# Kernel optimization log

Hardware: AMD Instinct MI355X
Metric: run time of the kernel (lower is better)

Reference implementation:

```python
import jax, jax.numpy as jnp
import numpy as np

NODES = 23   # 22 players + ball per frame-graph
K = 8        # random neighbors per node
B, T = 64, 128
G = B * T            # total graphs (frames)
N = G * NODES        # total nodes
D_IN, H, RH = 16, 128, 128


def setup_inputs() -> dict:
    key = jax.random.key(0)
    ks = jax.random.split(key, 10)
    x = jax.random.normal(ks[0], (N, D_IN), jnp.float32)
    # per-graph random edges: dst = each node repeated K times, src = random node in same graph
    src_local = jax.random.randint(ks[1], (G, NODES * K), 0, NODES)
    dst_local = jnp.tile(jnp.repeat(jnp.arange(NODES), K)[None, :], (G, 1))
    off = (jnp.arange(G) * NODES)[:, None]
    edge_index = jnp.stack([(src_local + off).reshape(-1),
                            (dst_local + off).reshape(-1)]).astype(jnp.int32)
    runner_idx = jax.random.randint(ks[2], (G,), 0, NODES, dtype=jnp.int32)
    sc = lambda k, sh: (jax.random.normal(k, sh, jnp.float32) * 0.05)
    return {
        'x': x, 'edge_index': edge_index, 'runner_idx': runner_idx,
        'W1': sc(ks[3], (D_IN, H)), 'b1': jnp.zeros((H,), jnp.float32),
        'W2': sc(ks[4], (H, H)),    'b2': jnp.zeros((H,), jnp.float32),
        'W_ih': sc(ks[5], (3 * RH, H)), 'W_hh': sc(ks[6], (3 * RH, RH)),
        'b_ih': jnp.zeros((3 * RH,), jnp.float32), 'b_hh': jnp.zeros((3 * RH,), jnp.float32),
        'Wp': sc(ks[7], (RH, 2)), 'bp': jnp.zeros((2,), jnp.float32),
    }


def _gcn_conv(h, edge_index, W, b):
    # PyG GCNConv: add self-loops, symmetric normalization, scatter-sum
    h = h @ W
    loop = jnp.arange(N, dtype=edge_index.dtype)
    s = jnp.concatenate([edge_index[0], loop])
    d = jnp.concatenate([edge_index[1], loop])
    deg = jax.ops.segment_sum(jnp.ones_like(s, h.dtype), d, num_segments=N)
    dinv = jnp.where(deg > 0, jax.lax.rsqrt(deg), 0.0)
    norm = dinv[s] * dinv[d]                      # [E+N]
    out = jax.ops.segment_sum(h[s] * norm[:, None], d, num_segments=N)
    return out + b


def _gru(seq, W_ih, W_hh, b_ih, b_hh):
    # torch GRU: gates in r,z,n order
    xg = seq @ W_ih.T + b_ih                      # [B,T,3RH]
    def step(hprev, xt):
        gh = hprev @ W_hh.T + b_hh
        xr, xz, xn = jnp.split(xt, 3, axis=-1)
        hr, hz, hn = jnp.split(gh, 3, axis=-1)
        r = jax.nn.sigmoid(xr + hr)
        z = jax.nn.sigmoid(xz + hz)
        n = jnp.tanh(xn + r * hn)
        hnew = (1.0 - z) * n + z * hprev
        return hnew, hnew
    h0 = jnp.zeros((seq.shape[0], RH), seq.dtype)
    _, outs = jax.lax.scan(step, h0, jnp.swapaxes(xg, 0, 1))
    return jnp.swapaxes(outs, 0, 1)               # [B,T,RH]


def reference(x, edge_index, runner_idx, W1, b1, W2, b2,
              W_ih, W_hh, b_ih, b_hh, Wp, bp):
    h = jax.nn.relu(_gcn_conv(x, edge_index, W1, b1))
    h = jax.nn.relu(_gcn_conv(h, edge_index, W2, b2))
    # fused equivalent of the per-graph nonzero()/indexing loop:
    runner_global = jnp.arange(G, dtype=jnp.int32) * NODES + runner_idx
    seq = h[runner_global].reshape(B, T, H)       # all lengths == T, padding is a no-op
    out = _gru(seq, W_ih, W_hh, b_ih, b_hh)
    return out @ Wp + bp                          # [B,T,2]
```

## Files before the change

### kernel.cpp

```cpp
#include <hip/hip_runtime.h>
#include <hip/hip_bf16.h>
#include <math.h>

#define GG 8192
#define NODESN 23
#define KK 8
#define DIN 16
#define HH 128
#define RHH 128
#define EPG (NODESN*KK)
#define TTT 128
#define BBB 64
#define HPAD 132

#define GRU_BARRIER() asm volatile("s_waitcnt lgkmcnt(0)\n\ts_barrier" ::: "memory")

__global__ __launch_bounds__(256) void gcn_fused(
    const float* __restrict__ x, const int* __restrict__ esrc,
    const int* __restrict__ runner,
    const float* __restrict__ W1, const float* __restrict__ b1,
    const float* __restrict__ W2, const float* __restrict__ b2,
    float* __restrict__ seq)
{
    __shared__ float xs[NODESN * DIN];
    __shared__ float W1s[DIN * HH];
    __shared__ int   srcs[EPG];
    __shared__ float t1[NODESN * HH];
    __shared__ float b1s[HH];
    __shared__ float hsum[HH];
    __shared__ float red[256];

    const int g = blockIdx.x;
    const int tid = threadIdx.x;

    for (int i = tid; i < NODESN * DIN; i += 256) xs[i] = x[g * NODESN * DIN + i];
    for (int i = tid; i < DIN * HH; i += 256)     W1s[i] = W1[i];
    for (int i = tid; i < EPG; i += 256)          srcs[i] = esrc[g * EPG + i] - g * NODESN;
    if (tid < HH) b1s[tid] = b1[tid];
    __syncthreads();

    for (int idx = tid; idx < NODESN * HH; idx += 256) {
        int n = idx >> 7, j = idx & 127;
        float acc = 0.f;
        #pragma unroll
        for (int k = 0; k < DIN; k += 4) {
            float4 xv = *(const float4*)&xs[n * DIN + k];
            acc = fmaf(xv.x, W1s[(k+0)*HH + j],
                  fmaf(xv.y, W1s[(k+1)*HH + j],
                  fmaf(xv.z, W1s[(k+2)*HH + j],
                  fmaf(xv.w, W1s[(k+3)*HH + j], acc))));
        }
        t1[idx] = acc;
    }
    __syncthreads();

    const int r = runner[g];
    {
        const int j = tid & 127, sgrp = tid >> 7;
        float part = 0.f;
        for (int slot = sgrp; slot < 9; slot += 2) {
            int node = (slot < 8) ? srcs[r * KK + slot] : r;
            float acc = t1[node * HH + j];
            #pragma unroll
            for (int k = 0; k < KK; k++) acc += t1[srcs[node * KK + k] * HH + j];
            part += fmaxf(acc * (1.f / 9.f) + b1s[j], 0.f);
        }
        red[tid] = part;
    }
    __syncthreads();
    if (tid < HH) hsum[tid] = red[tid] + red[tid + 128];
    __syncthreads();

    {
        const int j = tid & 127, kh = tid >> 7;
        float acc = 0.f;
        #pragma unroll
        for (int kq = 0; kq < 16; kq++) {
            int k = kh * 64 + kq * 4;
            float4 hv = *(const float4*)&hsum[k];
            acc = fmaf(hv.x, W2[(k+0)*HH + j],
                  fmaf(hv.y, W2[(k+1)*HH + j],
                  fmaf(hv.z, W2[(k+2)*HH + j],
                  fmaf(hv.w, W2[(k+3)*HH + j], acc))));
        }
        red[tid] = acc;
    }
    __syncthreads();
    if (tid < HH)
        seq[(size_t)g * HH + tid] =
            fmaxf((red[tid] + red[tid + 128]) * (1.f / 9.f) + b2[tid], 0.f);
}

__global__ void transpose_wih(const float* __restrict__ W, float* __restrict__ WT)
{
    int idx = blockIdx.x * 256 + threadIdx.x;
    if (idx < 3 * RHH * RHH) {
        int jj = idx / RHH, kk = idx - jj * RHH;
        WT[kk * (3 * RHH) + jj] = W[idx];
    }
}

__global__ __launch_bounds__(384) void xg_kernel(
    const float* __restrict__ seq, const float* __restrict__ WT,
    const float* __restrict__ b_ih, float* __restrict__ xg)
{
    const int tid = threadIdx.x;
    const int m0 = blockIdx.x * 8;
    const float* srow = seq + (size_t)m0 * RHH;
    float acc[8];
    const float bv = b_ih[tid];
    #pragma unroll
    for (int mi = 0; mi < 8; mi++) acc[mi] = bv;
    for (int k = 0; k < RHH; k += 4) {
        float w0 = WT[(k+0)*384 + tid];
        float w1 = WT[(k+1)*384 + tid];
        float w2 = WT[(k+2)*384 + tid];
        float w3 = WT[(k+3)*384 + tid];
        #pragma unroll
        for (int mi = 0; mi < 8; mi++) {
            float4 sv = *(const float4*)(srow + mi * RHH + k);
            acc[mi] = fmaf(sv.x, w0, fmaf(sv.y, w1, fmaf(sv.z, w2, fmaf(sv.w, w3, acc[mi]))));
        }
    }
    #pragma unroll
    for (int mi = 0; mi < 8; mi++)
        xg[(size_t)(m0 + mi) * 384 + tid] = acc[mi];
}

__global__ __launch_bounds__(512, 2) void gru_kernel(
    const float* __restrict__ xg, const float* __restrict__ W_hh,
    const float* __restrict__ b_hh, const float* __restrict__ Wp,
    const float* __restrict__ bp, float* __restrict__ out)
{
    __shared__ float h_hist[(TTT + 1) * HPAD];
    __shared__ float xg_s[2][3 * RHH];

    const int b   = blockIdx.x;
    const int tid = threadIdx.x;
    const int i   = tid >> 2;
    const int q   = tid & 3;

    float wr[32], wz[32], wn[32];
    int loff[8];
    {
        const float* br = W_hh + (size_t)i * RHH + q * 32;
        const float* bz = br + (size_t)RHH * RHH;
        const float* bn = bz + (size_t)RHH * RHH;
        #pragma unroll
        for (int m = 0; m < 8; m++) {
            int p = (m + 2 * q) & 7;
            loff[m] = q * 32 + 4 * p;
            float4 v;
            v = *(const float4*)(br + 4*p); wr[4*m]=v.x; wr[4*m+1]=v.y; wr[4*m+2]=v.z; wr[4*m+3]=v.w;
            v = *(const float4*)(bz + 4*p); wz[4*m]=v.x; wz[4*m+1]=v.y; wz[4*m+2]=v.z; wz[4*m+3]=v.w;
            v = *(const float4*)(bn + 4*p); wn[4*m]=v.x; wn[4*m+1]=v.y; wn[4*m+2]=v.z; wn[4*m+3]=v.w;
        }
    }
    float bhr = 0.f, bhz = 0.f, bhn = 0.f;
    if (q == 0) { bhr = b_hh[i]; bhz = b_hh[RHH + i]; bhn = b_hh[2 * RHH + i]; }

    if (tid < RHH) h_hist[tid] = 0.f;
    const float* xbase = xg + (size_t)b * TTT * 3 * RHH;
    float xnext = 0.f;
    if (tid < 3 * RHH) {
        xg_s[0][tid] = xbase[tid];
        xnext = xbase[3 * RHH + tid];
    }
    float hprev = 0.f;
    __syncthreads();

    for (int t = 0; t < TTT; t++) {
        const float* hrow = &h_hist[t * HPAD];
        float ar0 = 0.f, ar1 = 0.f, az0 = 0.f, az1 = 0.f, an0 = 0.f, an1 = 0.f;
        #pragma unroll
        for (int m = 0; m < 8; m++) {
            float4 hv = *(const float4*)(hrow + loff[m]);
            if (m & 1) {
                ar1 = fmaf(hv.x, wr[4*m], fmaf(hv.y, wr[4*m+1], fmaf(hv.z, wr[4*m+2], fmaf(hv.w, wr[4*m+3], ar1))));
                az1 = fmaf(hv.x, wz[4*m], fmaf(hv.y, wz[4*m+1], fmaf(hv.z, wz[4*m+2], fmaf(hv.w, wz[4*m+3], az1))));
                an1 = fmaf(hv.x, wn[4*m], fmaf(hv.y, wn[4*m+1], fmaf(hv.z, wn[4*m+2], fmaf(hv.w, wn[4*m+3], an1))));
            } else {
                ar0 = fmaf(hv.x, wr[4*m], fmaf(hv.y, wr[4*m+1], fmaf(hv.z, wr[4*m+2], fmaf(hv.w, wr[4*m+3], ar0))));
                az0 = fmaf(hv.x, wz[4*m], fmaf(hv.y, wz[4*m+1], fmaf(hv.z, wz[4*m+2], fmaf(hv.w, wz[4*m+3], az0))));
                an0 = fmaf(hv.x, wn[4*m], fmaf(hv.y, wn[4*m+1], fmaf(hv.z, wn[4*m+2], fmaf(hv.w, wn[4*m+3], an0))));
            }
        }
        float ar = ar0 + ar1, az = az0 + az1, an = an0 + an1;

        if (tid < 3 * RHH) {
            xg_s[(t + 1) & 1][tid] = xnext;
            xnext = (t + 2 < TTT) ? xbase[(size_t)(t + 2) * 3 * RHH + tid] : 0.f;
        }

        ar += __shfl_xor(ar, 1); ar += __shfl_xor(ar, 2);
        az += __shfl_xor(az, 1); az += __shfl_xor(az, 2);
        an += __shfl_xor(an, 1); an += __shfl_xor(an, 2);

        if (q == 0) {
            const float* xr_s = xg_s[t & 1];
            float xr = xr_s[i], xz = xr_s[RHH + i], xn = xr_s[2 * RHH + i];
            float sr = xr + ar + bhr;
            float sz = xz + az + bhz;
            float rg = 1.f / (1.f + __expf(-sr));
            float zg = 1.f / (1.f + __expf(-sz));
            float tv = fmaf(rg, an + bhn, xn);
            tv = fminf(fmaxf(tv, -15.f), 15.f);
            float e2 = __expf(-2.f * tv);
            float ng = (1.f - e2) / (1.f + e2);
            hprev = fmaf(zg, hprev, (1.f - zg) * ng);
            h_hist[(t + 1) * HPAD + i] = hprev;
        }
        GRU_BARRIER();
    }

    if (tid < 2 * RHH) xg_s[0][tid] = Wp[tid];
    if (tid < 2)       xg_s[1][tid] = bp[tid];
    __syncthreads();

    #pragma unroll
    for (int pass = 0; pass < 2; pass++) {
        int t = (tid >> 3) + pass * 64;
        int c = (tid >> 2) & 1;
        int s = tid & 3;
        (void)s;
        int s2 = tid & 3;
        float acc = 0.f;
        const float* hr = &h_hist[(t + 1) * HPAD + s2 * 32];
        #pragma unroll
        for (int ii = 0; ii < 32; ii += 4) {
            float4 hv = *(const float4*)(hr + ii);
            int k = s2 * 32 + ii;
            acc = fmaf(hv.x, xg_s[0][(k+0)*2 + c],
                  fmaf(hv.y, xg_s[0][(k+1)*2 + c],
                  fmaf(hv.z, xg_s[0][(k+2)*2 + c],
                  fmaf(hv.w, xg_s[0][(k+3)*2 + c], acc))));
        }
        acc += __shfl_xor(acc, 1);
        acc += __shfl_xor(acc, 2);
        if (s2 == 0)
            out[((size_t)b * TTT + t) * 2 + c] = acc + xg_s[1][c];
    }
}

extern "C" void kernel_launch(void* const* d_in, const int* in_sizes, int n_in,
                              void* d_out, int out_size, void* d_ws, size_t ws_size,
                              hipStream_t stream)
{
    const float* x      = (const float*)d_in[0];
    const int*   eidx   = (const int*)d_in[1];
    const int*   runner = (const int*)d_in[2];
    const float* W1     = (const float*)d_in[3];
    const float* b1     = (const float*)d_in[4];
    const float* W2     = (const float*)d_in[5];
    const float* b2     = (const float*)d_in[6];
    const float* W_ih   = (const float*)d_in[7];
    const float* W_hh   = (const float*)d_in[8];
    const float* b_ih   = (const float*)d_in[9];
    const float* b_hh   = (const float*)d_in[10];
    const float* Wp     = (const float*)d_in[11];
    const float* bp     = (const float*)d_in[12];
    float* out = (float*)d_out;

    float* seq = (float*)d_ws;
    float* xg  = seq + (size_t)GG * HH;
    float* WT  = xg + (size_t)GG * 3 * RHH;

    transpose_wih<<<192, 256, 0, stream>>>(W_ih, WT);
    gcn_fused<<<GG, 256, 0, stream>>>(x, eidx, runner, W1, b1, W2, b2, seq);
    xg_kernel<<<GG / 8, 384, 0, stream>>>(seq, WT, b_ih, xg);
    gru_kernel<<<BBB, 512, 0, stream>>>(xg, W_hh, b_hh, Wp, bp, out);
}
```

Baseline: 264.8 us.

## Split GCN W2 matmul into batched kernel and widen GRU to 1024 threads

The per-graph W2 matvec moves out of the GCN kernel into a separate batched kernel that reuses each W2 load across 16 graphs, and W1 is held in registers instead of shared memory. The GRU kernel now runs 1024 threads, with 8 lanes per hidden unit, so each thread holds half as many W_hh weights and the serial per-step dot product is shorter, at the cost of an extra shuffle stage. The extra launch adds a global round trip for the aggregated node sums, which reuse the xg buffer as scratch.

```diff
diff --git a/kernel.cpp b/kernel.cpp
--- a/kernel.cpp
+++ b/kernel.cpp
@@ -15,80 +15,90 @@
 
 #define GRU_BARRIER() asm volatile("s_waitcnt lgkmcnt(0)\n\ts_barrier" ::: "memory")
 
-__global__ __launch_bounds__(256) void gcn_fused(
+__global__ __launch_bounds__(256) void gcn_hsum(
     const float* __restrict__ x, const int* __restrict__ esrc,
     const int* __restrict__ runner,
     const float* __restrict__ W1, const float* __restrict__ b1,
-    const float* __restrict__ W2, const float* __restrict__ b2,
-    float* __restrict__ seq)
+    float* __restrict__ hsum_g)
 {
     __shared__ float xs[NODESN * DIN];
-    __shared__ float W1s[DIN * HH];
     __shared__ int   srcs[EPG];
     __shared__ float t1[NODESN * HH];
-    __shared__ float b1s[HH];
-    __shared__ float hsum[HH];
     __shared__ float red[256];
 
-    const int g = blockIdx.x;
-    const int tid = threadIdx.x;
+    const int g   = blockIdx.x;
+    const int tid = threadIdx.x;
+    const int j   = tid & 127;
+    const int nh  = tid >> 7;
 
     for (int i = tid; i < NODESN * DIN; i += 256) xs[i] = x[g * NODESN * DIN + i];
-    for (int i = tid; i < DIN * HH; i += 256)     W1s[i] = W1[i];
     for (int i = tid; i < EPG; i += 256)          srcs[i] = esrc[g * EPG + i] - g * NODESN;
-    if (tid < HH) b1s[tid] = b1[tid];
-    __syncthreads();
-
-    for (int idx = tid; idx < NODESN * HH; idx += 256) {
-        int n = idx >> 7, j = idx & 127;
+
+    float w[DIN];
+    #pragma unroll
+    for (int k = 0; k < DIN; k++) w[k] = W1[k * HH + j];
+    const float b1j = b1[j];
+    __syncthreads();
+
+    const int n0 = nh * 12;
+    const int n1 = nh ? NODESN : 12;
+    for (int n = n0; n < n1; n++) {
         float acc = 0.f;
         #pragma unroll
         for (int k = 0; k < DIN; k += 4) {
             float4 xv = *(const float4*)&xs[n * DIN + k];
-            acc = fmaf(xv.x, W1s[(k+0)*HH + j],
-                  fmaf(xv.y, W1s[(k+1)*HH + j],
-                  fmaf(xv.z, W1s[(k+2)*HH + j],
-                  fmaf(xv.w, W1s[(k+3)*HH + j], acc))));
-        }
-        t1[idx] = acc;
+            acc = fmaf(xv.x, w[k], fmaf(xv.y, w[k+1], fmaf(xv.z, w[k+2], fmaf(xv.w, w[k+3], acc))));
+        }
+        t1[n * HH + j] = acc;
     }
     __syncthreads();
 
     const int r = runner[g];
-    {
-        const int j = tid & 127, sgrp = tid >> 7;
-        float part = 0.f;
-        for (int slot = sgrp; slot < 9; slot += 2) {
-            int node = (slot < 8) ? srcs[r * KK + slot] : r;
-            float acc = t1[node * HH + j];
-            #pragma unroll
-            for (int k = 0; k < KK; k++) acc += t1[srcs[node * KK + k] * HH + j];
-            part += fmaxf(acc * (1.f / 9.f) + b1s[j], 0.f);
-        }
-        red[tid] = part;
-    }
-    __syncthreads();
-    if (tid < HH) hsum[tid] = red[tid] + red[tid + 128];
-    __syncthreads();
-
-    {
-        const int j = tid & 127, kh = tid >> 7;
-        float acc = 0.f;
-        #pragma unroll
-        for (int kq = 0; kq < 16; kq++) {
-            int k = kh * 64 + kq * 4;
-            float4 hv = *(const float4*)&hsum[k];
-            acc = fmaf(hv.x, W2[(k+0)*HH + j],
-                  fmaf(hv.y, W2[(k+1)*HH + j],
-                  fmaf(hv.z, W2[(k+2)*HH + j],
-                  fmaf(hv.w, W2[(k+3)*HH + j], acc))));
-        }
-        red[tid] = acc;
-    }
-    __syncthreads();
-    if (tid < HH)
-        seq[(size_t)g * HH + tid] =
-            fmaxf((red[tid] + red[tid + 128]) * (1.f / 9.f) + b2[tid], 0.f);
+    float part = 0.f;
+    for (int slot = nh; slot < 9; slot += 2) {
+        int node = (slot < 8) ? srcs[r * KK + slot] : r;
+        float acc = t1[node * HH + j];
+        #pragma unroll
+        for (int k = 0; k < KK; k++) acc += t1[srcs[node * KK + k] * HH + j];
+        part += fmaxf(acc * (1.f / 9.f) + b1j, 0.f);
+    }
+    red[tid] = part;
+    __syncthreads();
+    if (tid < HH) hsum_g[(size_t)g * HH + tid] = red[tid] + red[tid + 128];
+}
+
+__global__ __launch_bounds__(256) void seq_kernel(
+    const float* __restrict__ hsum_g, const float* __restrict__ W2,
+    const float* __restrict__ b2, float* __restrict__ seq)
+{
+    __shared__ float hs[16 * HH];
+    const int tid = threadIdx.x;
+    const int j = tid & 127, mh = tid >> 7;
+    const size_t base = (size_t)blockIdx.x * 16 * HH;
+
+    for (int v = tid; v < 16 * HH / 4; v += 256)
+        ((float4*)hs)[v] = ((const float4*)(hsum_g + base))[v];
+    __syncthreads();
+
+    float acc[8];
+    #pragma unroll
+    for (int m = 0; m < 8; m++) acc[m] = 0.f;
+    const float* hrow = hs + mh * 8 * HH;
+    for (int k = 0; k < HH; k += 4) {
+        float w0  = W2[(k+0)*HH + j];
+        float w1  = W2[(k+1)*HH + j];
+        float w2v = W2[(k+2)*HH + j];
+        float w3  = W2[(k+3)*HH + j];
+        #pragma unroll
+        for (int m = 0; m < 8; m++) {
+            float4 hv = *(const float4*)&hrow[m * HH + k];
+            acc[m] = fmaf(hv.x, w0, fmaf(hv.y, w1, fmaf(hv.z, w2v, fmaf(hv.w, w3, acc[m]))));
+        }
+    }
+    const float bj = b2[j];
+    #pragma unroll
+    for (int m = 0; m < 8; m++)
+        seq[base + (size_t)(mh * 8 + m) * HH + j] = fmaxf(acc[m] * (1.f/9.f) + bj, 0.f);
 }
 
 __global__ void transpose_wih(const float* __restrict__ W, float* __restrict__ WT)
@@ -127,7 +137,7 @@
         xg[(size_t)(m0 + mi) * 384 + tid] = acc[mi];
 }
 
-__global__ __launch_bounds__(512, 2) void gru_kernel(
+__global__ __launch_bounds__(1024, 4) void gru_kernel(
     const float* __restrict__ xg, const float* __restrict__ W_hh,
     const float* __restrict__ b_hh, const float* __restrict__ Wp,
     const float* __restrict__ bp, float* __restrict__ out)
@@ -137,25 +147,33 @@
 
     const int b   = blockIdx.x;
     const int tid = threadIdx.x;
-    const int i   = tid >> 2;
-    const int q   = tid & 3;
-
-    float wr[32], wz[32], wn[32];
-    int loff[8];
+    const int i   = tid >> 3;
+    const int q   = tid & 7;
+
+    float wr[16], wz[16], wn[16];
+    int loff[4];
     {
-        const float* br = W_hh + (size_t)i * RHH + q * 32;
+        const float* br = W_hh + (size_t)i * RHH;
         const float* bz = br + (size_t)RHH * RHH;
         const float* bn = bz + (size_t)RHH * RHH;
         #pragma unroll
-        for (int m = 0; m < 8; m++) {
-            int p = (m + 2 * q) & 7;
-            loff[m] = q * 32 + 4 * p;
+        for (int m = 0; m < 4; m++) {
+            int p = (m + (q >> 1)) & 3;
+            int o = q * 16 + 4 * p;
+            loff[m] = o;
             float4 v;
-            v = *(const float4*)(br + 4*p); wr[4*m]=v.x; wr[4*m+1]=v.y; wr[4*m+2]=v.z; wr[4*m+3]=v.w;
-            v = *(const float4*)(bz + 4*p); wz[4*m]=v.x; wz[4*m+1]=v.y; wz[4*m+2]=v.z; wz[4*m+3]=v.w;
-            v = *(const float4*)(bn + 4*p); wn[4*m]=v.x; wn[4*m+1]=v.y; wn[4*m+2]=v.z; wn[4*m+3]=v.w;
-        }
-    }
+            v = *(const float4*)(br + o); wr[4*m]=v.x; wr[4*m+1]=v.y; wr[4*m+2]=v.z; wr[4*m+3]=v.w;
+            v = *(const float4*)(bz + o); wz[4*m]=v.x; wz[4*m+1]=v.y; wz[4*m+2]=v.z; wz[4*m+3]=v.w;
+            v = *(const float4*)(bn + o); wn[4*m]=v.x; wn[4*m+1]=v.y; wn[4*m+2]=v.z; wn[4*m+3]=v.w;
+        }
+    }
+    #pragma unroll
+    for (int m = 0; m < 16; m++) {
+        asm volatile("" : "+v"(wr[m]));
+        asm volatile("" : "+v"(wz[m]));
+        asm volatile("" : "+v"(wn[m]));
+    }
+
     float bhr = 0.f, bhz = 0.f, bhn = 0.f;
     if (q == 0) { bhr = b_hh[i]; bhz = b_hh[RHH + i]; bhn = b_hh[2 * RHH + i]; }
 
@@ -171,30 +189,23 @@
 
     for (int t = 0; t < TTT; t++) {
         const float* hrow = &h_hist[t * HPAD];
-        float ar0 = 0.f, ar1 = 0.f, az0 = 0.f, az1 = 0.f, an0 = 0.f, an1 = 0.f;
-        #pragma unroll
-        for (int m = 0; m < 8; m++) {
+        float ar = 0.f, az = 0.f, an = 0.f;
+        #pragma unroll
+        for (int m = 0; m < 4; m++) {
             float4 hv = *(const float4*)(hrow + loff[m]);
-            if (m & 1) {
-                ar1 = fmaf(hv.x, wr[4*m], fmaf(hv.y, wr[4*m+1], fmaf(hv.z, wr[4*m+2], fmaf(hv.w, wr[4*m+3], ar1))));
-                az1 = fmaf(hv.x, wz[4*m], fmaf(hv.y, wz[4*m+1], fmaf(hv.z, wz[4*m+2], fmaf(hv.w, wz[4*m+3], az1))));
-                an1 = fmaf(hv.x, wn[4*m], fmaf(hv.y, wn[4*m+1], fmaf(hv.z, wn[4*m+2], fmaf(hv.w, wn[4*m+3], an1))));
-            } else {
-                ar0 = fmaf(hv.x, wr[4*m], fmaf(hv.y, wr[4*m+1], fmaf(hv.z, wr[4*m+2], fmaf(hv.w, wr[4*m+3], ar0))));
-                az0 = fmaf(hv.x, wz[4*m], fmaf(hv.y, wz[4*m+1], fmaf(hv.z, wz[4*m+2], fmaf(hv.w, wz[4*m+3], az0))));
-                an0 = fmaf(hv.x, wn[4*m], fmaf(hv.y, wn[4*m+1], fmaf(hv.z, wn[4*m+2], fmaf(hv.w, wn[4*m+3], an0))));
-            }
-        }
-        float ar = ar0 + ar1, az = az0 + az1, an = an0 + an1;
+            ar = fmaf(hv.x, wr[4*m], fmaf(hv.y, wr[4*m+1], fmaf(hv.z, wr[4*m+2], fmaf(hv.w, wr[4*m+3], ar))));
+            az = fmaf(hv.x, wz[4*m], fmaf(hv.y, wz[4*m+1], fmaf(hv.z, wz[4*m+2], fmaf(hv.w, wz[4*m+3], az))));
+            an = fmaf(hv.x, wn[4*m], fmaf(hv.y, wn[4*m+1], fmaf(hv.z, wn[4*m+2], fmaf(hv.w, wn[4*m+3], an))));
+        }
 
         if (tid < 3 * RHH) {
             xg_s[(t + 1) & 1][tid] = xnext;
             xnext = (t + 2 < TTT) ? xbase[(size_t)(t + 2) * 3 * RHH + tid] : 0.f;
         }
 
-        ar += __shfl_xor(ar, 1); ar += __shfl_xor(ar, 2);
-        az += __shfl_xor(az, 1); az += __shfl_xor(az, 2);
-        an += __shfl_xor(an, 1); an += __shfl_xor(an, 2);
+        ar += __shfl_xor(ar, 1); ar += __shfl_xor(ar, 2); ar += __shfl_xor(ar, 4);
+        az += __shfl_xor(az, 1); az += __shfl_xor(az, 2); az += __shfl_xor(az, 4);
+        an += __shfl_xor(an, 1); an += __shfl_xor(an, 2); an += __shfl_xor(an, 4);
 
         if (q == 0) {
             const float* xr_s = xg_s[t & 1];
@@ -217,19 +228,16 @@
     if (tid < 2)       xg_s[1][tid] = bp[tid];
     __syncthreads();
 
-    #pragma unroll
-    for (int pass = 0; pass < 2; pass++) {
-        int t = (tid >> 3) + pass * 64;
-        int c = (tid >> 2) & 1;
-        int s = tid & 3;
-        (void)s;
-        int s2 = tid & 3;
+    {
+        const int s = tid & 3;
+        const int c = (tid >> 2) & 1;
+        const int t = tid >> 3;
         float acc = 0.f;
-        const float* hr = &h_hist[(t + 1) * HPAD + s2 * 32];
+        const float* hr = &h_hist[(t + 1) * HPAD + s * 32];
         #pragma unroll
         for (int ii = 0; ii < 32; ii += 4) {
             float4 hv = *(const float4*)(hr + ii);
-            int k = s2 * 32 + ii;
+            int k = s * 32 + ii;
             acc = fmaf(hv.x, xg_s[0][(k+0)*2 + c],
                   fmaf(hv.y, xg_s[0][(k+1)*2 + c],
                   fmaf(hv.z, xg_s[0][(k+2)*2 + c],
@@ -237,7 +245,7 @@
         }
         acc += __shfl_xor(acc, 1);
         acc += __shfl_xor(acc, 2);
-        if (s2 == 0)
+        if (s == 0)
             out[((size_t)b * TTT + t) * 2 + c] = acc + xg_s[1][c];
     }
 }
@@ -261,12 +269,14 @@
     const float* bp     = (const float*)d_in[12];
     float* out = (float*)d_out;
 
-    float* seq = (float*)d_ws;
-    float* xg  = seq + (size_t)GG * HH;
-    float* WT  = xg + (size_t)GG * 3 * RHH;
+    float* seq    = (float*)d_ws;
+    float* xg     = seq + (size_t)GG * HH;
+    float* WT     = xg + (size_t)GG * 3 * RHH;
+    float* hsum_g = xg;
 
     transpose_wih<<<192, 256, 0, stream>>>(W_ih, WT);
-    gcn_fused<<<GG, 256, 0, stream>>>(x, eidx, runner, W1, b1, W2, b2, seq);
+    gcn_hsum<<<GG, 256, 0, stream>>>(x, eidx, runner, W1, b1, hsum_g);
+    seq_kernel<<<GG / 16, 256, 0, stream>>>(hsum_g, W2, b2, seq);
     xg_kernel<<<GG / 8, 384, 0, stream>>>(seq, WT, b_ih, xg);
-    gru_kernel<<<BBB, 512, 0, stream>>>(xg, W_hh, b_hh, Wp, bp, out);
-}
+    gru_kernel<<<BBB, 1024, 0, stream>>>(xg, W_hh, b_hh, Wp, bp, out);
+}
```

Result: no change. 264.9 us (+0.0%).
